# Optimization experiments

Measured on AMD Instinct MI355X. Metric: run time of the kernel, lower is better.

Reference implementation:

```python
import jax, jax.numpy as jnp
import numpy as np

N_NODES = 50000
N_EDGES = 800000
IN_DIM = 128
HID = 32
HEADS = 4
OUT_DIM = 2
NEG_SLOPE = 0.2


def gat_conv(feat, W, al, ar, bias, src, dst, n_nodes):
    """DGL GATConv (eval mode, no dropout). feat: [N, Fin]; W: [Fin, H*D];
    al, ar: [H, D]; bias: [H*D]. Returns [N, H, D]."""
    H, D = al.shape
    hf = (feat @ W).reshape(n_nodes, H, D)              # [N,H,D]
    el = jnp.einsum('nhd,hd->nh', hf, al)               # [N,H]
    er = jnp.einsum('nhd,hd->nh', hf, ar)               # [N,H]
    e = el[src] + er[dst]                               # [E,H]
    e = jax.nn.leaky_relu(e, NEG_SLOPE)
    # segment softmax over incoming edges of each dst node
    emax = jax.ops.segment_max(e, dst, num_segments=n_nodes)  # [N,H]
    emax = jnp.where(jnp.isfinite(emax), emax, 0.0)
    ex = jnp.exp(e - emax[dst])                         # [E,H]
    denom = jax.ops.segment_sum(ex, dst, num_segments=n_nodes)  # [N,H]
    alpha = ex / jnp.maximum(denom[dst], 1e-30)         # [E,H]
    msg = hf[src] * alpha[:, :, None]                   # [E,H,D]
    out = jax.ops.segment_sum(msg, dst, num_segments=n_nodes)   # [N,H,D]
    return out + bias.reshape(1, H, D)


def setup_inputs() -> dict:
    key = jax.random.key(0)
    ks = jax.random.split(key, 16)
    f32 = jnp.float32
    in_feat = jax.random.normal(ks[0], (N_NODES, IN_DIM), dtype=f32)
    src = jax.random.randint(ks[1], (N_EDGES,), 0, N_NODES)
    dst = jax.random.randint(ks[2], (N_EDGES,), 0, N_NODES)
    s1 = 1.0 / np.sqrt(IN_DIM)
    s2 = 1.0 / np.sqrt(HID * HEADS)
    W1 = jax.random.normal(ks[3], (IN_DIM, HEADS * HID), dtype=f32) * s1
    al1 = jax.random.normal(ks[4], (HEADS, HID), dtype=f32) * 0.1
    ar1 = jax.random.normal(ks[5], (HEADS, HID), dtype=f32) * 0.1
    b1 = jnp.zeros((HEADS * HID,), dtype=f32)
    W2 = jax.random.normal(ks[6], (HEADS * HID, HEADS * HID), dtype=f32) * s2
    al2 = jax.random.normal(ks[7], (HEADS, HID), dtype=f32) * 0.1
    ar2 = jax.random.normal(ks[8], (HEADS, HID), dtype=f32) * 0.1
    b2 = jnp.zeros((HEADS * HID,), dtype=f32)
    Wout = jax.random.normal(ks[9], (HID, OUT_DIM), dtype=f32) * (1.0 / np.sqrt(HID))
    bout = jnp.zeros((OUT_DIM,), dtype=f32)
    return {"in_feat": in_feat, "W1": W1, "al1": al1, "ar1": ar1, "b1": b1,
            "W2": W2, "al2": al2, "ar2": ar2, "b2": b2,
            "Wout": Wout, "bout": bout, "src": src, "dst": dst}


def reference(in_feat, W1, al1, ar1, b1, W2, al2, ar2, b2, Wout, bout, src, dst):
    h = gat_conv(in_feat, W1, al1, ar1, b1, src, dst, N_NODES)  # [N,H,D]
    h = jax.nn.relu(h.reshape(N_NODES, HEADS * HID))            # flatten(1) + relu
    h = gat_conv(h, W2, al2, ar2, b2, src, dst, N_NODES)        # [N,H,D]
    emd = h.mean(axis=1)                                        # mean over heads -> [N,D]
    logits = jax.nn.relu(emd) @ Wout + bout                     # [N,2]
    return jax.nn.softmax(logits, axis=-1)
```

## Files before the change

### kernel.cpp

```cpp
#include <hip/hip_runtime.h>
#include <cmath>

#define N_NODES 50000
#define N_EDGES 800000
#define NBUCK 196
#define NHB 196
#define EPB 4096

typedef unsigned short u16;
typedef unsigned int u32;
typedef __attribute__((ext_vector_type(8))) short bf16x8;
typedef __attribute__((ext_vector_type(4))) float f32x4;

static __device__ __forceinline__ float lrelu(float x) { return x > 0.f ? x : 0.2f * x; }
static __device__ __forceinline__ float bf2f(u16 u) { return __uint_as_float(((u32)u) << 16); }
static __device__ __forceinline__ u16 f2bf(float f) {
    u32 b = __float_as_uint(f);
    return (u16)((b + 0x7FFFu + ((b >> 16) & 1u)) >> 16);
}
static __device__ __forceinline__ u32 pack2(float a, float b) {
    return (u32)f2bf(a) | ((u32)f2bf(b) << 16);
}
static __device__ __forceinline__ float sx(u32 u, int k) {
    return (float)((int)(u << ((3 - k) * 8)) >> 24);
}

__global__ __launch_bounds__(1024) void bhist_pack_k(const int* __restrict__ dst, u32* __restrict__ bcnt,
                                                     const float* __restrict__ W1, const float* __restrict__ W2,
                                                     u16* __restrict__ Wp1, u16* __restrict__ Wp2) {
    int tid = threadIdx.x;
    if (blockIdx.x < NHB) {
        __shared__ u32 hist[NBUCK];
        for (int i = tid; i < NBUCK; i += 1024) hist[i] = 0;
        __syncthreads();
        int base = blockIdx.x * EPB;
#pragma unroll
        for (int k = 0; k < 4; ++k) {
            int e = base + k * 1024 + tid;
            if (e < N_EDGES) atomicAdd(&hist[dst[e] >> 8], 1u);
        }
        __syncthreads();
        for (int i = tid; i < NBUCK; i += 1024) bcnt[(size_t)i * NHB + blockIdx.x] = hist[i];
    } else {
        int gi = (blockIdx.x - NHB) * 1024 + tid;
        const float* W = (gi < 16384) ? W1 : W2;
        u16* Wp = (gi < 16384) ? Wp1 : Wp2;
        int i = gi & 16383;
        int j = i & 7, lane = (i >> 3) & 63, ks = (i >> 9) & 3, nt = i >> 11;
        int k = ks * 32 + (lane >> 4) * 8 + j;
        int ncol = nt * 16 + (lane & 15);
        Wp[i] = f2bf(W[k * 128 + ncol]);
    }
}

__global__ __launch_bounds__(256) void scant_k(const u32* __restrict__ bcnt, u32* __restrict__ wbase,
                                               u32* __restrict__ btot) {
    __shared__ u32 s[256];
    int i = blockIdx.x, t = threadIdx.x;
    u32 v = (t < NHB) ? bcnt[(size_t)i * NHB + t] : 0;
    s[t] = v;
    __syncthreads();
    for (int o = 1; o < 256; o <<= 1) {
        u32 x = (t >= o) ? s[t - o] : 0;
        __syncthreads();
        s[t] += x;
        __syncthreads();
    }
    if (t < NHB) wbase[(size_t)i * NHB + t] = s[t] - v;
    if (t == 255) btot[i] = s[255];
}

__global__ __launch_bounds__(256) void scanb2_k(const u32* __restrict__ btot, int* __restrict__ bstart) {
    __shared__ u32 s[256];
    int t = threadIdx.x;
    u32 v = (t < NBUCK) ? btot[t] : 0;
    s[t] = v;
    __syncthreads();
    for (int o = 1; o < 256; o <<= 1) {
        u32 x = (t >= o) ? s[t - o] : 0;
        __syncthreads();
        s[t] += x;
        __syncthreads();
    }
    if (t < NBUCK) bstart[t] = (int)(s[t] - v);
    if (t == NBUCK - 1) bstart[NBUCK] = (int)s[t];
}

__global__ __launch_bounds__(1024) void bscatter_k(const int* __restrict__ src, const int* __restrict__ dst,
                                                   const u32* __restrict__ wbase, const int* __restrict__ bstart,
                                                   u32* __restrict__ bucketed) {
    __shared__ u32 pos[NBUCK];
    int tid = threadIdx.x;
    for (int i = tid; i < NBUCK; i += 1024)
        pos[i] = (u32)bstart[i] + wbase[(size_t)i * NHB + blockIdx.x];
    __syncthreads();
    int base = blockIdx.x * EPB;
#pragma unroll
    for (int k = 0; k < 4; ++k) {
        int e = base + k * 1024 + tid;
        if (e < N_EDGES) {
            int d = dst[e];
            int b = d >> 8;
            u32 p = atomicAdd(&pos[b], 1u);
            bucketed[p] = (u32)src[e] | ((u32)(d & 255) << 16);
        }
    }
}

__global__ __launch_bounds__(256) void bcsr_k(const u32* __restrict__ bucketed, const int* __restrict__ bstart,
                                              int* __restrict__ offs, u16* __restrict__ srcs) {
    __shared__ u32 cnt[256];
    __shared__ int s[256];
    __shared__ u32 fp[256];
    int b = blockIdx.x;
    int tid = threadIdx.x;
    int ebeg = bstart[b], eend = bstart[b + 1];
    int ne = eend - ebeg;
    cnt[tid] = 0;
    __syncthreads();
    for (int i = tid; i < ne; i += 256)
        atomicAdd(&cnt[bucketed[ebeg + i] >> 16], 1u);
    __syncthreads();
    s[tid] = (int)cnt[tid];
    __syncthreads();
    for (int o = 1; o < 256; o <<= 1) {
        int v = (tid >= o) ? s[tid - o] : 0;
        __syncthreads();
        s[tid] += v;
        __syncthreads();
    }
    int excl = s[tid] - (int)cnt[tid];
    int node = b * 256 + tid;
    if (node < N_NODES) offs[node] = ebeg + excl;
    if (b == NBUCK - 1 && tid == 0) offs[N_NODES] = N_EDGES;
    fp[tid] = (u32)excl;
    __syncthreads();
    for (int i = tid; i < ne; i += 256) {
        u32 u = bucketed[ebeg + i];
        u32 p = atomicAdd(&fp[u >> 16], 1u);
        srcs[ebeg + p] = (u16)(u & 0xFFFFu);
    }
}

template <int BF16IN>
__global__ __launch_bounds__(256) void gemm_mfma(
    const void* __restrict__ Xv, const u16* __restrict__ Wp,
    const float* __restrict__ al, const float* __restrict__ ar,
    signed char* __restrict__ hq, float2* __restrict__ elhs, float* __restrict__ er, int n)
{
    __shared__ u16 xs[64][136];
    int row0 = blockIdx.x * 64;
    int tid = threadIdx.x;
    if (BF16IN) {
        const uint4* Xb = (const uint4*)Xv;
        for (int i = tid; i < 1024; i += 256) {
            int r = i >> 4, c = i & 15;
            uint4 v = make_uint4(0u, 0u, 0u, 0u);
            if (row0 + r < n) v = Xb[(size_t)(row0 + r) * 16 + c];
            ((uint4*)&xs[r][0])[c] = v;
        }
    } else {
        const float4* X4 = (const float4*)Xv;
        for (int i = tid; i < 2048; i += 256) {
            int r = i >> 5, c = i & 31;
            float4 v = make_float4(0.f, 0.f, 0.f, 0.f);
            if (row0 + r < n) v = X4[(size_t)(row0 + r) * 32 + c];
            ((uint2*)&xs[r][0])[c] = make_uint2(pack2(v.x, v.y), pack2(v.z, v.w));
        }
    }
    __syncthreads();

    int wave = tid >> 6, lane = tid & 63;
    int quad = lane >> 4, l15 = lane & 15;

    bf16x8 bfrag[2][4];
#pragma unroll
    for (int ct = 0; ct < 2; ++ct) {
        int nt = wave * 2 + ct;
#pragma unroll
        for (int ks = 0; ks < 4; ++ks)
            bfrag[ct][ks] = *(const bf16x8*)(Wp + ((((nt * 4 + ks) * 64) + lane) << 3));
    }

    f32x4 acc[4][2];
#pragma unroll
    for (int rt = 0; rt < 4; ++rt)
#pragma unroll
        for (int ct = 0; ct < 2; ++ct)
            acc[rt][ct] = (f32x4){0.f, 0.f, 0.f, 0.f};

#pragma unroll
    for (int ks = 0; ks < 4; ++ks) {
#pragma unroll
        for (int rt = 0; rt < 4; ++rt) {
            bf16x8 a = *(const bf16x8*)&xs[rt * 16 + l15][ks * 32 + quad * 8];
            acc[rt][0] = __builtin_amdgcn_mfma_f32_16x16x32_bf16(a, bfrag[0][ks], acc[rt][0], 0, 0, 0);
            acc[rt][1] = __builtin_amdgcn_mfma_f32_16x16x32_bf16(a, bfrag[1][ks], acc[rt][1], 0, 0, 0);
        }
    }

    float alv0 = al[wave * 32 + l15], alv1 = al[wave * 32 + 16 + l15];
    float arv0 = ar[wave * 32 + l15], arv1 = ar[wave * 32 + 16 + l15];
#pragma unroll
    for (int rt = 0; rt < 4; ++rt) {
#pragma unroll
        for (int r = 0; r < 4; ++r) {
            int row = row0 + rt * 16 + quad * 4 + r;
            float c0 = acc[rt][0][r], c1 = acc[rt][1][r];
            float m = fmaxf(fabsf(c0), fabsf(c1));
            m = fmaxf(m, __shfl_xor(m, 1));
            m = fmaxf(m, __shfl_xor(m, 2));
            m = fmaxf(m, __shfl_xor(m, 4));
            m = fmaxf(m, __shfl_xor(m, 8));
            m = fmaxf(m, 1e-20f);
            float qsc = 127.0f / m;
            if (row < n) {
                hq[(size_t)row * 128 + wave * 32 + l15] = (signed char)(int)rintf(c0 * qsc);
                hq[(size_t)row * 128 + wave * 32 + 16 + l15] = (signed char)(int)rintf(c1 * qsc);
            }
            float pel = c0 * alv0 + c1 * alv1;
            float per = c0 * arv0 + c1 * arv1;
            pel += __shfl_xor(pel, 1); pel += __shfl_xor(pel, 2);
            pel += __shfl_xor(pel, 4); pel += __shfl_xor(pel, 8);
            per += __shfl_xor(per, 1); per += __shfl_xor(per, 2);
            per += __shfl_xor(per, 4); per += __shfl_xor(per, 8);
            if (l15 == 0 && row < n) {
                elhs[row * 4 + wave] = make_float2(pel, m * (1.0f / 127.0f));
                er[row * 4 + wave] = per;
            }
        }
    }
}

static __device__ __forceinline__ void agg_core(
    int node, int lane, const int* __restrict__ offs, const u16* __restrict__ srcs,
    const float2* __restrict__ elhs, const float* __restrict__ er,
    const signed char* __restrict__ hq,
    float acc[8], float& den)
{
    int qw = lane >> 4;
    int q = lane & 15;
    int h = q >> 2;
    float erh = er[node * 4 + h];
    int beg = offs[node], end = offs[node + 1];
    int deg = end - beg;
    den = 0.f;
#pragma unroll
    for (int i = 0; i < 8; i++) acc[i] = 0.f;

    if (deg <= 64) {
        int psrc = (lane < deg) ? (int)srcs[beg + lane] : 0;
        int base = beg;
        for (; base + 16 <= end; base += 16) {
            int j = base - beg + qw;
            int ss[4];
            ss[0] = __shfl(psrc, j);
            ss[1] = __shfl(psrc, j + 4);
            ss[2] = __shfl(psrc, j + 8);
            ss[3] = __shfl(psrc, j + 12);
            float2 eh[4];
            uint2 uv[4];
#pragma unroll
            for (int k = 0; k < 4; ++k) {
                eh[k] = elhs[ss[k] * 4 + h];
                uv[k] = *(const uint2*)(hq + (size_t)ss[k] * 128 + q * 8);
            }
#pragma unroll
            for (int k = 0; k < 4; ++k) {
                float w = __expf(lrelu(eh[k].x + erh));
                float ws = w * eh[k].y;
                den += w;
                acc[0] += ws * sx(uv[k].x, 0);
                acc[1] += ws * sx(uv[k].x, 1);
                acc[2] += ws * sx(uv[k].x, 2);
                acc[3] += ws * sx(uv[k].x, 3);
                acc[4] += ws * sx(uv[k].y, 0);
                acc[5] += ws * sx(uv[k].y, 1);
                acc[6] += ws * sx(uv[k].y, 2);
                acc[7] += ws * sx(uv[k].y, 3);
            }
        }
        for (; base + 8 <= end; base += 8) {
            int j = base - beg + qw;
            int s0 = __shfl(psrc, j);
            int s1 = __shfl(psrc, j + 4);
            float2 e0 = elhs[s0 * 4 + h], e1 = elhs[s1 * 4 + h];
            uint2 u0 = *(const uint2*)(hq + (size_t)s0 * 128 + q * 8);
            uint2 u1 = *(const uint2*)(hq + (size_t)s1 * 128 + q * 8);
            float w0 = __expf(lrelu(e0.x + erh));
            float w1 = __expf(lrelu(e1.x + erh));
            float ws0 = w0 * e0.y, ws1 = w1 * e1.y;
            den += w0 + w1;
            acc[0] += ws0 * sx(u0.x, 0) + ws1 * sx(u1.x, 0);
            acc[1] += ws0 * sx(u0.x, 1) + ws1 * sx(u1.x, 1);
            acc[2] += ws0 * sx(u0.x, 2) + ws1 * sx(u1.x, 2);
            acc[3] += ws0 * sx(u0.x, 3) + ws1 * sx(u1.x, 3);
            acc[4] += ws0 * sx(u0.y, 0) + ws1 * sx(u1.y, 0);
            acc[5] += ws0 * sx(u0.y, 1) + ws1 * sx(u1.y, 1);
            acc[6] += ws0 * sx(u0.y, 2) + ws1 * sx(u1.y, 2);
            acc[7] += ws0 * sx(u0.y, 3) + ws1 * sx(u1.y, 3);
        }
        for (; base < end; base += 4) {
            int e = base + qw;
            bool valid = e < end;
            int j = valid ? (e - beg) : 0;
            int s = __shfl(psrc, j);
            float2 eh = elhs[s * 4 + h];
            float w = valid ? __expf(lrelu(eh.x + erh)) : 0.f;
            float ws = w * eh.y;
            uint2 u = *(const uint2*)(hq + (size_t)s * 128 + q * 8);
            den += w;
            acc[0] += ws * sx(u.x, 0);
            acc[1] += ws * sx(u.x, 1);
            acc[2] += ws * sx(u.x, 2);
            acc[3] += ws * sx(u.x, 3);
            acc[4] += ws * sx(u.y, 0);
            acc[5] += ws * sx(u.y, 1);
            acc[6] += ws * sx(u.y, 2);
            acc[7] += ws * sx(u.y, 3);
        }
    } else {
        for (int base = beg; base < end; base += 4) {
            int e = base + qw;
            bool valid = e < end;
            int ec = valid ? e : end - 1;
            int s = srcs[ec];
            float2 eh = elhs[s * 4 + h];
            float w = valid ? __expf(lrelu(eh.x + erh)) : 0.f;
            float ws = w * eh.y;
            uint2 u = *(const uint2*)(hq + (size_t)s * 128 + q * 8);
            den += w;
            acc[0] += ws * sx(u.x, 0);
            acc[1] += ws * sx(u.x, 1);
            acc[2] += ws * sx(u.x, 2);
            acc[3] += ws * sx(u.x, 3);
            acc[4] += ws * sx(u.y, 0);
            acc[5] += ws * sx(u.y, 1);
            acc[6] += ws * sx(u.y, 2);
            acc[7] += ws * sx(u.y, 3);
        }
    }
#pragma unroll
    for (int i = 0; i < 8; i++) {
        acc[i] += __shfl_xor(acc[i], 16);
        acc[i] += __shfl_xor(acc[i], 32);
    }
    den += __shfl_xor(den, 16);
    den += __shfl_xor(den, 32);
}

__global__ __launch_bounds__(256) void agg1_k(const int* __restrict__ offs, const u16* __restrict__ srcs,
                                              const float2* __restrict__ elhs, const float* __restrict__ er,
                                              const signed char* __restrict__ hq,
                                              const float* __restrict__ bias, u16* __restrict__ h1) {
    int node = blockIdx.x * 4 + (threadIdx.x >> 6);
    int lane = threadIdx.x & 63;
    if (node >= N_NODES) return;
    float acc[8], den;
    agg_core(node, lane, offs, srcs, elhs, er, hq, acc, den);
    int qw = lane >> 4, q = lane & 15;
    if (qw == 0) {
        float inv = 1.0f / fmaxf(den, 1e-30f);
        float o[8];
#pragma unroll
        for (int i = 0; i < 8; i++)
            o[i] = fmaxf(acc[i] * inv + bias[q * 8 + i], 0.f);
        uint4 pk;
        pk.x = pack2(o[0], o[1]);
        pk.y = pack2(o[2], o[3]);
        pk.z = pack2(o[4], o[5]);
        pk.w = pack2(o[6], o[7]);
        *(uint4*)(h1 + (size_t)node * 128 + q * 8) = pk;
    }
}

__global__ __launch_bounds__(256) void agg2_k(const int* __restrict__ offs, const u16* __restrict__ srcs,
                                              const float2* __restrict__ elhs, const float* __restrict__ er,
                                              const signed char* __restrict__ hq,
                                              const float* __restrict__ bias,
                                              const float* __restrict__ Wout, const float* __restrict__ bout,
                                              float2* __restrict__ out) {
    int node = blockIdx.x * 4 + (threadIdx.x >> 6);
    int lane = threadIdx.x & 63;
    if (node >= N_NODES) return;
    float acc[8], den;
    agg_core(node, lane, offs, srcs, elhs, er, hq, acc, den);
    int q = lane & 15;
    float inv = 1.0f / fmaxf(den, 1e-30f);
    float o[8];
#pragma unroll
    for (int i = 0; i < 8; i++) o[i] = acc[i] * inv + bias[q * 8 + i];
#pragma unroll
    for (int i = 0; i < 8; i++) {
        o[i] += __shfl_xor(o[i], 4);
        o[i] += __shfl_xor(o[i], 8);
        o[i] = fmaxf(0.25f * o[i], 0.f);
    }
    int d0 = (q & 3) * 8;
    float l0 = 0.f, l1 = 0.f;
#pragma unroll
    for (int i = 0; i < 8; i++) {
        l0 += o[i] * Wout[(d0 + i) * 2];
        l1 += o[i] * Wout[(d0 + i) * 2 + 1];
    }
    l0 += __shfl_xor(l0, 1); l0 += __shfl_xor(l0, 2);
    l1 += __shfl_xor(l1, 1); l1 += __shfl_xor(l1, 2);
    if (lane == 0) {
        l0 += bout[0];
        l1 += bout[1];
        float mx = fmaxf(l0, l1);
        float e0 = __expf(l0 - mx), e1 = __expf(l1 - mx);
        float invs = 1.f / (e0 + e1);
        out[node] = make_float2(e0 * invs, e1 * invs);
    }
}

extern "C" void kernel_launch(void* const* d_in, const int* in_sizes, int n_in,
                              void* d_out, int out_size, void* d_ws, size_t ws_size,
                              hipStream_t stream) {
    const float* in_feat = (const float*)d_in[0];
    const float* W1   = (const float*)d_in[1];
    const float* al1  = (const float*)d_in[2];
    const float* ar1  = (const float*)d_in[3];
    const float* b1   = (const float*)d_in[4];
    const float* W2   = (const float*)d_in[5];
    const float* al2  = (const float*)d_in[6];
    const float* ar2  = (const float*)d_in[7];
    const float* b2   = (const float*)d_in[8];
    const float* Wout = (const float*)d_in[9];
    const float* bout = (const float*)d_in[10];
    const int*   src  = (const int*)d_in[11];
    const int*   dst  = (const int*)d_in[12];
    float* out = (float*)d_out;

    char* ws = (char*)d_ws;
    size_t off = 0;
    auto carve = [&](size_t bytes) {
        char* p = ws + off;
        off = (off + bytes + 255) & ~(size_t)255;
        return p;
    };
    signed char* hq  = (signed char*)carve((size_t)N_NODES * 128);
    float2* elhs     = (float2*)carve((size_t)N_NODES * 4 * 8);
    u16*   h1        = (u16*)carve((size_t)N_NODES * 128 * 2);
    float* er        = (float*)carve((size_t)N_NODES * 4 * 4);
    u16*   srcs      = (u16*)carve((size_t)N_EDGES * 2);
    u32*   bucketed  = (u32*)carve((size_t)N_EDGES * 4);
    u32*   bcnt      = (u32*)carve((size_t)NBUCK * NHB * 4);
    u32*   wbase     = (u32*)carve((size_t)NBUCK * NHB * 4);
    u32*   btot      = (u32*)carve((size_t)NBUCK * 4);
    int*   bstart    = (int*)carve((size_t)(NBUCK + 1) * 4);
    int*   offs      = (int*)carve((size_t)(N_NODES + 1) * 4);
    u16*   Wp1       = (u16*)carve((size_t)16384 * 2);
    u16*   Wp2       = (u16*)carve((size_t)16384 * 2);
    (void)ws_size; (void)in_sizes; (void)n_in; (void)out_size;

    const int GB = (N_NODES + 63) / 64;
    const int AB = (N_NODES + 3) / 4;

    bhist_pack_k<<<NHB + 32, 1024, 0, stream>>>(dst, bcnt, W1, W2, Wp1, Wp2);
    scant_k<<<NBUCK, 256, 0, stream>>>(bcnt, wbase, btot);
    scanb2_k<<<1, 256, 0, stream>>>(btot, bstart);
    bscatter_k<<<NHB, 1024, 0, stream>>>(src, dst, wbase, bstart, bucketed);
    bcsr_k<<<NBUCK, 256, 0, stream>>>(bucketed, bstart, offs, srcs);

    gemm_mfma<0><<<GB, 256, 0, stream>>>(in_feat, Wp1, al1, ar1, hq, elhs, er, N_NODES);
    agg1_k<<<AB, 256, 0, stream>>>(offs, srcs, elhs, er, hq, b1, h1);

    gemm_mfma<1><<<GB, 256, 0, stream>>>(h1, Wp2, al2, ar2, hq, elhs, er, N_NODES);
    agg2_k<<<AB, 256, 0, stream>>>(offs, srcs, elhs, er, hq, b2, Wout, bout, (float2*)out);
}
```

Before: 212.8 us.

## Fuse layer-1 aggregation with layer-2 GEMM and merge scan kernels

Layer-1 aggregation now writes its 64-node tile of bf16 activations into shared memory, and the same block runs the layer-2 MFMA GEMM, int8 quantisation and attention-logit computation. This removes the h1 global round trip and one kernel launch. Separately, the two-level bucket scan is merged into one kernel using a last-block-done atomic counter, which drops another launch. The cost is fewer blocks (one per 64 nodes instead of one per 4) during the gather-heavy aggregation phase, which lowers the parallelism available to hide latency.

```diff
diff --git a/kernel.cpp b/kernel.cpp
--- a/kernel.cpp
+++ b/kernel.cpp
@@ -27,7 +27,8 @@
 
 __global__ __launch_bounds__(1024) void bhist_pack_k(const int* __restrict__ dst, u32* __restrict__ bcnt,
                                                      const float* __restrict__ W1, const float* __restrict__ W2,
-                                                     u16* __restrict__ Wp1, u16* __restrict__ Wp2) {
+                                                     u16* __restrict__ Wp1, u16* __restrict__ Wp2,
+                                                     u32* __restrict__ done) {
     int tid = threadIdx.x;
     if (blockIdx.x < NHB) {
         __shared__ u32 hist[NBUCK];
@@ -42,6 +43,7 @@
         __syncthreads();
         for (int i = tid; i < NBUCK; i += 1024) bcnt[(size_t)i * NHB + blockIdx.x] = hist[i];
     } else {
+        if (blockIdx.x == NHB && tid == 0) *done = 0;
         int gi = (blockIdx.x - NHB) * 1024 + tid;
         const float* W = (gi < 16384) ? W1 : W2;
         u16* Wp = (gi < 16384) ? Wp1 : Wp2;
@@ -54,8 +56,10 @@
 }
 
 __global__ __launch_bounds__(256) void scant_k(const u32* __restrict__ bcnt, u32* __restrict__ wbase,
-                                               u32* __restrict__ btot) {
+                                               u32* __restrict__ btot, int* __restrict__ bstart,
+                                               u32* __restrict__ done) {
     __shared__ u32 s[256];
+    __shared__ bool amLast;
     int i = blockIdx.x, t = threadIdx.x;
     u32 v = (t < NHB) ? bcnt[(size_t)i * NHB + t] : 0;
     s[t] = v;
@@ -67,14 +71,14 @@
         __syncthreads();
     }
     if (t < NHB) wbase[(size_t)i * NHB + t] = s[t] - v;
-    if (t == 255) btot[i] = s[255];
-}
-
-__global__ __launch_bounds__(256) void scanb2_k(const u32* __restrict__ btot, int* __restrict__ bstart) {
-    __shared__ u32 s[256];
-    int t = threadIdx.x;
-    u32 v = (t < NBUCK) ? btot[t] : 0;
-    s[t] = v;
+    if (t == 255) atomicExch(&btot[i], s[255]);
+    __threadfence();
+    if (t == 0) amLast = (atomicAdd(done, 1u) == NBUCK - 1);
+    __syncthreads();
+    if (!amLast) return;
+    __threadfence();
+    u32 v2 = (t < NBUCK) ? atomicAdd(&btot[t], 0u) : 0;
+    s[t] = v2;
     __syncthreads();
     for (int o = 1; o < 256; o <<= 1) {
         u32 x = (t >= o) ? s[t - o] : 0;
@@ -82,7 +86,7 @@
         s[t] += x;
         __syncthreads();
     }
-    if (t < NBUCK) bstart[t] = (int)(s[t] - v);
+    if (t < NBUCK) bstart[t] = (int)(s[t] - v2);
     if (t == NBUCK - 1) bstart[NBUCK] = (int)s[t];
 }
 
@@ -349,28 +353,104 @@
     den += __shfl_xor(den, 32);
 }
 
-__global__ __launch_bounds__(256) void agg1_k(const int* __restrict__ offs, const u16* __restrict__ srcs,
-                                              const float2* __restrict__ elhs, const float* __restrict__ er,
-                                              const signed char* __restrict__ hq,
-                                              const float* __restrict__ bias, u16* __restrict__ h1) {
-    int node = blockIdx.x * 4 + (threadIdx.x >> 6);
-    int lane = threadIdx.x & 63;
-    if (node >= N_NODES) return;
-    float acc[8], den;
-    agg_core(node, lane, offs, srcs, elhs, er, hq, acc, den);
-    int qw = lane >> 4, q = lane & 15;
-    if (qw == 0) {
-        float inv = 1.0f / fmaxf(den, 1e-30f);
-        float o[8];
-#pragma unroll
-        for (int i = 0; i < 8; i++)
-            o[i] = fmaxf(acc[i] * inv + bias[q * 8 + i], 0.f);
-        uint4 pk;
-        pk.x = pack2(o[0], o[1]);
-        pk.y = pack2(o[2], o[3]);
-        pk.z = pack2(o[4], o[5]);
-        pk.w = pack2(o[6], o[7]);
-        *(uint4*)(h1 + (size_t)node * 128 + q * 8) = pk;
+__global__ __launch_bounds__(256) void agg1_gemm2_k(
+    const int* __restrict__ offs, const u16* __restrict__ srcs,
+    const float2* __restrict__ elhs1, const float* __restrict__ er1,
+    const signed char* __restrict__ hq1, const float* __restrict__ b1,
+    const u16* __restrict__ Wp2, const float* __restrict__ al2, const float* __restrict__ ar2,
+    signed char* __restrict__ hq2, float2* __restrict__ elhs2, float* __restrict__ er2)
+{
+    __shared__ u16 xs[64][136];
+    int row0 = blockIdx.x * 64;
+    int tid = threadIdx.x;
+    int wave = tid >> 6, lane = tid & 63;
+    int q = lane & 15;
+
+    float bv[8];
+#pragma unroll
+    for (int i = 0; i < 8; i++) bv[i] = b1[q * 8 + i];
+
+    for (int it = 0; it < 16; ++it) {
+        int ln = wave * 16 + it;
+        int node = row0 + ln;
+        uint4 pk = make_uint4(0u, 0u, 0u, 0u);
+        if (node < N_NODES) {
+            float acc[8], den;
+            agg_core(node, lane, offs, srcs, elhs1, er1, hq1, acc, den);
+            if (lane < 16) {
+                float inv = 1.0f / fmaxf(den, 1e-30f);
+                float o[8];
+#pragma unroll
+                for (int i = 0; i < 8; i++)
+                    o[i] = fmaxf(acc[i] * inv + bv[i], 0.f);
+                pk.x = pack2(o[0], o[1]);
+                pk.y = pack2(o[2], o[3]);
+                pk.z = pack2(o[4], o[5]);
+                pk.w = pack2(o[6], o[7]);
+            }
+        }
+        if (lane < 16) ((uint4*)&xs[ln][0])[q] = pk;
+    }
+    __syncthreads();
+
+    int quad = lane >> 4, l15 = lane & 15;
+
+    bf16x8 bfrag[2][4];
+#pragma unroll
+    for (int ct = 0; ct < 2; ++ct) {
+        int nt = wave * 2 + ct;
+#pragma unroll
+        for (int ks = 0; ks < 4; ++ks)
+            bfrag[ct][ks] = *(const bf16x8*)(Wp2 + ((((nt * 4 + ks) * 64) + lane) << 3));
+    }
+
+    f32x4 acc2[4][2];
+#pragma unroll
+    for (int rt = 0; rt < 4; ++rt)
+#pragma unroll
+        for (int ct = 0; ct < 2; ++ct)
+            acc2[rt][ct] = (f32x4){0.f, 0.f, 0.f, 0.f};
+
+#pragma unroll
+    for (int ks = 0; ks < 4; ++ks) {
+#pragma unroll
+        for (int rt = 0; rt < 4; ++rt) {
+            bf16x8 a = *(const bf16x8*)&xs[rt * 16 + l15][ks * 32 + quad * 8];
+            acc2[rt][0] = __builtin_amdgcn_mfma_f32_16x16x32_bf16(a, bfrag[0][ks], acc2[rt][0], 0, 0, 0);
+            acc2[rt][1] = __builtin_amdgcn_mfma_f32_16x16x32_bf16(a, bfrag[1][ks], acc2[rt][1], 0, 0, 0);
+        }
+    }
+
+    float alv0 = al2[wave * 32 + l15], alv1 = al2[wave * 32 + 16 + l15];
+    float arv0 = ar2[wave * 32 + l15], arv1 = ar2[wave * 32 + 16 + l15];
+#pragma unroll
+    for (int rt = 0; rt < 4; ++rt) {
+#pragma unroll
+        for (int r = 0; r < 4; ++r) {
+            int row = row0 + rt * 16 + quad * 4 + r;
+            float c0 = acc2[rt][0][r], c1 = acc2[rt][1][r];
+            float m = fmaxf(fabsf(c0), fabsf(c1));
+            m = fmaxf(m, __shfl_xor(m, 1));
+            m = fmaxf(m, __shfl_xor(m, 2));
+            m = fmaxf(m, __shfl_xor(m, 4));
+            m = fmaxf(m, __shfl_xor(m, 8));
+            m = fmaxf(m, 1e-20f);
+            float qsc = 127.0f / m;
+            if (row < N_NODES) {
+                hq2[(size_t)row * 128 + wave * 32 + l15] = (signed char)(int)rintf(c0 * qsc);
+                hq2[(size_t)row * 128 + wave * 32 + 16 + l15] = (signed char)(int)rintf(c1 * qsc);
+            }
+            float pel = c0 * alv0 + c1 * alv1;
+            float per = c0 * arv0 + c1 * arv1;
+            pel += __shfl_xor(pel, 1); pel += __shfl_xor(pel, 2);
+            pel += __shfl_xor(pel, 4); pel += __shfl_xor(pel, 8);
+            per += __shfl_xor(per, 1); per += __shfl_xor(per, 2);
+            per += __shfl_xor(per, 4); per += __shfl_xor(per, 8);
+            if (l15 == 0 && row < N_NODES) {
+                elhs2[row * 4 + wave] = make_float2(pel, m * (1.0f / 127.0f));
+                er2[row * 4 + wave] = per;
+            }
+        }
     }
 }
 
@@ -442,8 +522,10 @@
     };
     signed char* hq  = (signed char*)carve((size_t)N_NODES * 128);
     float2* elhs     = (float2*)carve((size_t)N_NODES * 4 * 8);
-    u16*   h1        = (u16*)carve((size_t)N_NODES * 128 * 2);
     float* er        = (float*)carve((size_t)N_NODES * 4 * 4);
+    signed char* hq2 = (signed char*)carve((size_t)N_NODES * 128);
+    float2* elhs2    = (float2*)carve((size_t)N_NODES * 4 * 8);
+    float* er2       = (float*)carve((size_t)N_NODES * 4 * 4);
     u16*   srcs      = (u16*)carve((size_t)N_EDGES * 2);
     u32*   bucketed  = (u32*)carve((size_t)N_EDGES * 4);
     u32*   bcnt      = (u32*)carve((size_t)NBUCK * NHB * 4);
@@ -453,20 +535,20 @@
     int*   offs      = (int*)carve((size_t)(N_NODES + 1) * 4);
     u16*   Wp1       = (u16*)carve((size_t)16384 * 2);
     u16*   Wp2       = (u16*)carve((size_t)16384 * 2);
+    u32*   done      = (u32*)carve(256);
     (void)ws_size; (void)in_sizes; (void)n_in; (void)out_size;
 
     const int GB = (N_NODES + 63) / 64;
     const int AB = (N_NODES + 3) / 4;
 
-    bhist_pack_k<<<NHB + 32, 1024, 0, stream>>>(dst, bcnt, W1, W2, Wp1, Wp2);
-    scant_k<<<NBUCK, 256, 0, stream>>>(bcnt, wbase, btot);
-    scanb2_k<<<1, 256, 0, stream>>>(btot, bstart);
+    bhist_pack_k<<<NHB + 32, 1024, 0, stream>>>(dst, bcnt, W1, W2, Wp1, Wp2, done);
+    scant_k<<<NBUCK, 256, 0, stream>>>(bcnt, wbase, btot, bstart, done);
     bscatter_k<<<NHB, 1024, 0, stream>>>(src, dst, wbase, bstart, bucketed);
     bcsr_k<<<NBUCK, 256, 0, stream>>>(bucketed, bstart, offs, srcs);
 
     gemm_mfma<0><<<GB, 256, 0, stream>>>(in_feat, Wp1, al1, ar1, hq, elhs, er, N_NODES);
-    agg1_k<<<AB, 256, 0, stream>>>(offs, srcs, elhs, er, hq, b1, h1);
-
-    gemm_mfma<1><<<GB, 256, 0, stream>>>(h1, Wp2, al2, ar2, hq, elhs, er, N_NODES);
-    agg2_k<<<AB, 256, 0, stream>>>(offs, srcs, elhs, er, hq, b2, Wout, bout, (float2*)out);
-}
+
+    agg1_gemm2_k<<<GB, 256, 0, stream>>>(offs, srcs, elhs, er, hq, b1, Wp2, al2, ar2, hq2, elhs2, er2);
+
+    agg2_k<<<AB, 256, 0, stream>>>(offs, srcs, elhs2, er2, hq2, b2, Wout, bout, (float2*)out);
+}
```

Measured after the change: 239.4 us. +12.5%, slower.

## Fuse bucket scans via last-block pattern, widen CSR build, use biased uint8 features

Applied to the files above, without the earlier changes.

Merges the second-level bucket scan into the first scan kernel using an atomic counter so the last finishing block computes bucket starts, removing one launch. The CSR build kernel is widened to 1024 threads per bucket to process edges faster. Quantized features are stored as unsigned bytes with a +128 bias, decoded with a cheaper unsigned byte extract, and the bias is removed afterwards using an accumulated weight sum. This adds threadfence/atomic overhead and slight numerical change from bias subtraction.

```diff
diff --git a/kernel.cpp b/kernel.cpp
--- a/kernel.cpp
+++ b/kernel.cpp
@@ -9,11 +9,11 @@
 
 typedef unsigned short u16;
 typedef unsigned int u32;
+typedef unsigned char u8;
 typedef __attribute__((ext_vector_type(8))) short bf16x8;
 typedef __attribute__((ext_vector_type(4))) float f32x4;
 
 static __device__ __forceinline__ float lrelu(float x) { return x > 0.f ? x : 0.2f * x; }
-static __device__ __forceinline__ float bf2f(u16 u) { return __uint_as_float(((u32)u) << 16); }
 static __device__ __forceinline__ u16 f2bf(float f) {
     u32 b = __float_as_uint(f);
     return (u16)((b + 0x7FFFu + ((b >> 16) & 1u)) >> 16);
@@ -21,13 +21,14 @@
 static __device__ __forceinline__ u32 pack2(float a, float b) {
     return (u32)f2bf(a) | ((u32)f2bf(b) << 16);
 }
-static __device__ __forceinline__ float sx(u32 u, int k) {
-    return (float)((int)(u << ((3 - k) * 8)) >> 24);
+static __device__ __forceinline__ float ub(u32 u, int k) {
+    return (float)((u >> (k * 8)) & 0xffu);
 }
 
 __global__ __launch_bounds__(1024) void bhist_pack_k(const int* __restrict__ dst, u32* __restrict__ bcnt,
                                                      const float* __restrict__ W1, const float* __restrict__ W2,
-                                                     u16* __restrict__ Wp1, u16* __restrict__ Wp2) {
+                                                     u16* __restrict__ Wp1, u16* __restrict__ Wp2,
+                                                     u32* __restrict__ done) {
     int tid = threadIdx.x;
     if (blockIdx.x < NHB) {
         __shared__ u32 hist[NBUCK];
@@ -42,6 +43,7 @@
         __syncthreads();
         for (int i = tid; i < NBUCK; i += 1024) bcnt[(size_t)i * NHB + blockIdx.x] = hist[i];
     } else {
+        if (blockIdx.x == NHB && tid == 0) *done = 0;
         int gi = (blockIdx.x - NHB) * 1024 + tid;
         const float* W = (gi < 16384) ? W1 : W2;
         u16* Wp = (gi < 16384) ? Wp1 : Wp2;
@@ -54,8 +56,10 @@
 }
 
 __global__ __launch_bounds__(256) void scant_k(const u32* __restrict__ bcnt, u32* __restrict__ wbase,
-                                               u32* __restrict__ btot) {
+                                               u32* __restrict__ btot, int* __restrict__ bstart,
+                                               u32* __restrict__ done) {
     __shared__ u32 s[256];
+    __shared__ bool amLast;
     int i = blockIdx.x, t = threadIdx.x;
     u32 v = (t < NHB) ? bcnt[(size_t)i * NHB + t] : 0;
     s[t] = v;
@@ -67,14 +71,14 @@
         __syncthreads();
     }
     if (t < NHB) wbase[(size_t)i * NHB + t] = s[t] - v;
-    if (t == 255) btot[i] = s[255];
-}
-
-__global__ __launch_bounds__(256) void scanb2_k(const u32* __restrict__ btot, int* __restrict__ bstart) {
-    __shared__ u32 s[256];
-    int t = threadIdx.x;
-    u32 v = (t < NBUCK) ? btot[t] : 0;
-    s[t] = v;
+    if (t == 255) atomicExch(&btot[i], s[255]);
+    __threadfence();
+    if (t == 0) amLast = (atomicAdd(done, 1u) == NBUCK - 1);
+    __syncthreads();
+    if (!amLast) return;
+    __threadfence();
+    u32 v2 = (t < NBUCK) ? atomicAdd(&btot[t], 0u) : 0;
+    s[t] = v2;
     __syncthreads();
     for (int o = 1; o < 256; o <<= 1) {
         u32 x = (t >= o) ? s[t - o] : 0;
@@ -82,7 +86,7 @@
         s[t] += x;
         __syncthreads();
     }
-    if (t < NBUCK) bstart[t] = (int)(s[t] - v);
+    if (t < NBUCK) bstart[t] = (int)(s[t] - v2);
     if (t == NBUCK - 1) bstart[NBUCK] = (int)s[t];
 }
 
@@ -107,8 +111,8 @@
     }
 }
 
-__global__ __launch_bounds__(256) void bcsr_k(const u32* __restrict__ bucketed, const int* __restrict__ bstart,
-                                              int* __restrict__ offs, u16* __restrict__ srcs) {
+__global__ __launch_bounds__(1024) void bcsr_k(const u32* __restrict__ bucketed, const int* __restrict__ bstart,
+                                               int* __restrict__ offs, u16* __restrict__ srcs) {
     __shared__ u32 cnt[256];
     __shared__ int s[256];
     __shared__ u32 fp[256];
@@ -116,26 +120,28 @@
     int tid = threadIdx.x;
     int ebeg = bstart[b], eend = bstart[b + 1];
     int ne = eend - ebeg;
-    cnt[tid] = 0;
-    __syncthreads();
-    for (int i = tid; i < ne; i += 256)
+    if (tid < 256) cnt[tid] = 0;
+    __syncthreads();
+    for (int i = tid; i < ne; i += 1024)
         atomicAdd(&cnt[bucketed[ebeg + i] >> 16], 1u);
     __syncthreads();
-    s[tid] = (int)cnt[tid];
+    if (tid < 256) s[tid] = (int)cnt[tid];
     __syncthreads();
     for (int o = 1; o < 256; o <<= 1) {
-        int v = (tid >= o) ? s[tid - o] : 0;
-        __syncthreads();
-        s[tid] += v;
-        __syncthreads();
-    }
-    int excl = s[tid] - (int)cnt[tid];
-    int node = b * 256 + tid;
-    if (node < N_NODES) offs[node] = ebeg + excl;
+        int v = (tid < 256 && tid >= o) ? s[tid - o] : 0;
+        __syncthreads();
+        if (tid < 256) s[tid] += v;
+        __syncthreads();
+    }
+    if (tid < 256) {
+        int excl = s[tid] - (int)cnt[tid];
+        int node = b * 256 + tid;
+        if (node < N_NODES) offs[node] = ebeg + excl;
+        fp[tid] = (u32)excl;
+    }
     if (b == NBUCK - 1 && tid == 0) offs[N_NODES] = N_EDGES;
-    fp[tid] = (u32)excl;
-    __syncthreads();
-    for (int i = tid; i < ne; i += 256) {
+    __syncthreads();
+    for (int i = tid; i < ne; i += 1024) {
         u32 u = bucketed[ebeg + i];
         u32 p = atomicAdd(&fp[u >> 16], 1u);
         srcs[ebeg + p] = (u16)(u & 0xFFFFu);
@@ -146,7 +152,7 @@
 __global__ __launch_bounds__(256) void gemm_mfma(
     const void* __restrict__ Xv, const u16* __restrict__ Wp,
     const float* __restrict__ al, const float* __restrict__ ar,
-    signed char* __restrict__ hq, float2* __restrict__ elhs, float* __restrict__ er, int n)
+    u8* __restrict__ hq, float2* __restrict__ elhs, float* __restrict__ er, int n)
 {
     __shared__ u16 xs[64][136];
     int row0 = blockIdx.x * 64;
@@ -215,8 +221,8 @@
             m = fmaxf(m, 1e-20f);
             float qsc = 127.0f / m;
             if (row < n) {
-                hq[(size_t)row * 128 + wave * 32 + l15] = (signed char)(int)rintf(c0 * qsc);
-                hq[(size_t)row * 128 + wave * 32 + 16 + l15] = (signed char)(int)rintf(c1 * qsc);
+                hq[(size_t)row * 128 + wave * 32 + l15] = (u8)((int)rintf(c0 * qsc) + 128);
+                hq[(size_t)row * 128 + wave * 32 + 16 + l15] = (u8)((int)rintf(c1 * qsc) + 128);
             }
             float pel = c0 * alv0 + c1 * alv1;
             float per = c0 * arv0 + c1 * arv1;
@@ -235,7 +241,7 @@
 static __device__ __forceinline__ void agg_core(
     int node, int lane, const int* __restrict__ offs, const u16* __restrict__ srcs,
     const float2* __restrict__ elhs, const float* __restrict__ er,
-    const signed char* __restrict__ hq,
+    const u8* __restrict__ hq,
     float acc[8], float& den)
 {
     int qw = lane >> 4;
@@ -245,6 +251,7 @@
     int beg = offs[node], end = offs[node + 1];
     int deg = end - beg;
     den = 0.f;
+    float wss = 0.f;
 #pragma unroll
     for (int i = 0; i < 8; i++) acc[i] = 0.f;
 
@@ -270,14 +277,15 @@
                 float w = __expf(lrelu(eh[k].x + erh));
                 float ws = w * eh[k].y;
                 den += w;
-                acc[0] += ws * sx(uv[k].x, 0);
-                acc[1] += ws * sx(uv[k].x, 1);
-                acc[2] += ws * sx(uv[k].x, 2);
-                acc[3] += ws * sx(uv[k].x, 3);
-                acc[4] += ws * sx(uv[k].y, 0);
-                acc[5] += ws * sx(uv[k].y, 1);
-                acc[6] += ws * sx(uv[k].y, 2);
-                acc[7] += ws * sx(uv[k].y, 3);
+                wss += ws;
+                acc[0] += ws * ub(uv[k].x, 0);
+                acc[1] += ws * ub(uv[k].x, 1);
+                acc[2] += ws * ub(uv[k].x, 2);
+                acc[3] += ws * ub(uv[k].x, 3);
+                acc[4] += ws * ub(uv[k].y, 0);
+                acc[5] += ws * ub(uv[k].y, 1);
+                acc[6] += ws * ub(uv[k].y, 2);
+                acc[7] += ws * ub(uv[k].y, 3);
             }
         }
         for (; base + 8 <= end; base += 8) {
@@ -291,14 +299,15 @@
             float w1 = __expf(lrelu(e1.x + erh));
             float ws0 = w0 * e0.y, ws1 = w1 * e1.y;
             den += w0 + w1;
-            acc[0] += ws0 * sx(u0.x, 0) + ws1 * sx(u1.x, 0);
-            acc[1] += ws0 * sx(u0.x, 1) + ws1 * sx(u1.x, 1);
-            acc[2] += ws0 * sx(u0.x, 2) + ws1 * sx(u1.x, 2);
-            acc[3] += ws0 * sx(u0.x, 3) + ws1 * sx(u1.x, 3);
-            acc[4] += ws0 * sx(u0.y, 0) + ws1 * sx(u1.y, 0);
-            acc[5] += ws0 * sx(u0.y, 1) + ws1 * sx(u1.y, 1);
-            acc[6] += ws0 * sx(u0.y, 2) + ws1 * sx(u1.y, 2);
-            acc[7] += ws0 * sx(u0.y, 3) + ws1 * sx(u1.y, 3);
+            wss += ws0 + ws1;
+            acc[0] += ws0 * ub(u0.x, 0) + ws1 * ub(u1.x, 0);
+            acc[1] += ws0 * ub(u0.x, 1) + ws1 * ub(u1.x, 1);
+            acc[2] += ws0 * ub(u0.x, 2) + ws1 * ub(u1.x, 2);
+            acc[3] += ws0 * ub(u0.x, 3) + ws1 * ub(u1.x, 3);
+            acc[4] += ws0 * ub(u0.y, 0) + ws1 * ub(u1.y, 0);
+            acc[5] += ws0 * ub(u0.y, 1) + ws1 * ub(u1.y, 1);
+            acc[6] += ws0 * ub(u0.y, 2) + ws1 * ub(u1.y, 2);
+            acc[7] += ws0 * ub(u0.y, 3) + ws1 * ub(u1.y, 3);
         }
         for (; base < end; base += 4) {
             int e = base + qw;
@@ -310,14 +319,15 @@
             float ws = w * eh.y;
             uint2 u = *(const uint2*)(hq + (size_t)s * 128 + q * 8);
             den += w;
-            acc[0] += ws * sx(u.x, 0);
-            acc[1] += ws * sx(u.x, 1);
-            acc[2] += ws * sx(u.x, 2);
-            acc[3] += ws * sx(u.x, 3);
-            acc[4] += ws * sx(u.y, 0);
-            acc[5] += ws * sx(u.y, 1);
-            acc[6] += ws * sx(u.y, 2);
-            acc[7] += ws * sx(u.y, 3);
+            wss += ws;
+            acc[0] += ws * ub(u.x, 0);
+            acc[1] += ws * ub(u.x, 1);
+            acc[2] += ws * ub(u.x, 2);
+            acc[3] += ws * ub(u.x, 3);
+            acc[4] += ws * ub(u.y, 0);
+            acc[5] += ws * ub(u.y, 1);
+            acc[6] += ws * ub(u.y, 2);
+            acc[7] += ws * ub(u.y, 3);
         }
     } else {
         for (int base = beg; base < end; base += 4) {
@@ -330,14 +340,15 @@
             float ws = w * eh.y;
             uint2 u = *(const uint2*)(hq + (size_t)s * 128 + q * 8);
             den += w;
-            acc[0] += ws * sx(u.x, 0);
-            acc[1] += ws * sx(u.x, 1);
-            acc[2] += ws * sx(u.x, 2);
-            acc[3] += ws * sx(u.x, 3);
-            acc[4] += ws * sx(u.y, 0);
-            acc[5] += ws * sx(u.y, 1);
-            acc[6] += ws * sx(u.y, 2);
-            acc[7] += ws * sx(u.y, 3);
+            wss += ws;
+            acc[0] += ws * ub(u.x, 0);
+            acc[1] += ws * ub(u.x, 1);
+            acc[2] += ws * ub(u.x, 2);
+            acc[3] += ws * ub(u.x, 3);
+            acc[4] += ws * ub(u.y, 0);
+            acc[5] += ws * ub(u.y, 1);
+            acc[6] += ws * ub(u.y, 2);
+            acc[7] += ws * ub(u.y, 3);
         }
     }
 #pragma unroll
@@ -347,11 +358,15 @@
     }
     den += __shfl_xor(den, 16);
     den += __shfl_xor(den, 32);
+    wss += __shfl_xor(wss, 16);
+    wss += __shfl_xor(wss, 32);
+#pragma unroll
+    for (int i = 0; i < 8; i++) acc[i] -= 128.0f * wss;
 }
 
 __global__ __launch_bounds__(256) void agg1_k(const int* __restrict__ offs, const u16* __restrict__ srcs,
                                               const float2* __restrict__ elhs, const float* __restrict__ er,
-                                              const signed char* __restrict__ hq,
+                                              const u8* __restrict__ hq,
                                               const float* __restrict__ bias, u16* __restrict__ h1) {
     int node = blockIdx.x * 4 + (threadIdx.x >> 6);
     int lane = threadIdx.x & 63;
@@ -376,7 +391,7 @@
 
 __global__ __launch_bounds__(256) void agg2_k(const int* __restrict__ offs, const u16* __restrict__ srcs,
                                               const float2* __restrict__ elhs, const float* __restrict__ er,
-                                              const signed char* __restrict__ hq,
+                                              const u8* __restrict__ hq,
                                               const float* __restrict__ bias,
                                               const float* __restrict__ Wout, const float* __restrict__ bout,
                                               float2* __restrict__ out) {
@@ -440,10 +455,10 @@
         off = (off + bytes + 255) & ~(size_t)255;
         return p;
     };
-    signed char* hq  = (signed char*)carve((size_t)N_NODES * 128);
+    u8*    hq        = (u8*)carve((size_t)N_NODES * 128);
     float2* elhs     = (float2*)carve((size_t)N_NODES * 4 * 8);
+    float* er        = (float*)carve((size_t)N_NODES * 4 * 4);
     u16*   h1        = (u16*)carve((size_t)N_NODES * 128 * 2);
-    float* er        = (float*)carve((size_t)N_NODES * 4 * 4);
     u16*   srcs      = (u16*)carve((size_t)N_EDGES * 2);
     u32*   bucketed  = (u32*)carve((size_t)N_EDGES * 4);
     u32*   bcnt      = (u32*)carve((size_t)NBUCK * NHB * 4);
@@ -453,16 +468,16 @@
     int*   offs      = (int*)carve((size_t)(N_NODES + 1) * 4);
     u16*   Wp1       = (u16*)carve((size_t)16384 * 2);
     u16*   Wp2       = (u16*)carve((size_t)16384 * 2);
+    u32*   done      = (u32*)carve(256);
     (void)ws_size; (void)in_sizes; (void)n_in; (void)out_size;
 
     const int GB = (N_NODES + 63) / 64;
     const int AB = (N_NODES + 3) / 4;
 
-    bhist_pack_k<<<NHB + 32, 1024, 0, stream>>>(dst, bcnt, W1, W2, Wp1, Wp2);
-    scant_k<<<NBUCK, 256, 0, stream>>>(bcnt, wbase, btot);
-    scanb2_k<<<1, 256, 0, stream>>>(btot, bstart);
+    bhist_pack_k<<<NHB + 32, 1024, 0, stream>>>(dst, bcnt, W1, W2, Wp1, Wp2, done);
+    scant_k<<<NBUCK, 256, 0, stream>>>(bcnt, wbase, btot, bstart, done);
     bscatter_k<<<NHB, 1024, 0, stream>>>(src, dst, wbase, bstart, bucketed);
-    bcsr_k<<<NBUCK, 256, 0, stream>>>(bucketed, bstart, offs, srcs);
+    bcsr_k<<<NBUCK, 1024, 0, stream>>>(bucketed, bstart, offs, srcs);
 
     gemm_mfma<0><<<GB, 256, 0, stream>>>(in_feat, Wp1, al1, ar1, hq, elhs, er, N_NODES);
     agg1_k<<<AB, 256, 0, stream>>>(offs, srcs, elhs, er, hq, b1, h1);
```

Result: slower. 226.7 us (+6.5%).
